# Kernel tuning notes

Measured on AMD Instinct MI355X. Metric: run time of the kernel, lower is better.

## Reference

```python
import jax, jax.numpy as jnp
import numpy as np

T, D, E, K, F, SF = 4096, 1024, 8, 2, 1024, 1024  # tokens, d_model, experts, top_k, moe_ff, shared_ff


def setup_inputs() -> dict:
    key = jax.random.key(0)
    ks = jax.random.split(key, 10)
    hidden_states = jax.random.normal(ks[0], (T, D), jnp.float32)
    # balanced expert assignment: the fused kernel's get_split_sizes assumes tokens
    # split evenly across experts after permute_tokens, so exactly T*K/E per expert
    flat = jnp.arange(T * K) % E
    flat = jax.random.permutation(ks[1], flat)
    topk_indices = flat.reshape(T, K).astype(jnp.int32)
    w = jax.random.uniform(ks[2], (T, K), jnp.float32)
    topk_weights = w / w.sum(-1, keepdims=True)  # norm_topk_prob
    s = 0.02
    w_gate = jax.random.normal(ks[3], (E, D, F), jnp.float32) * s
    w_up = jax.random.normal(ks[4], (E, D, F), jnp.float32) * s
    w_down = jax.random.normal(ks[5], (E, F, D), jnp.float32) * s
    sw_gate = jax.random.normal(ks[6], (D, SF), jnp.float32) * s
    sw_up = jax.random.normal(ks[7], (D, SF), jnp.float32) * s
    sw_down = jax.random.normal(ks[8], (SF, D), jnp.float32) * s
    shared_gate_w = jax.random.normal(ks[9], (D, 1), jnp.float32) * s
    return dict(hidden_states=hidden_states, topk_weights=topk_weights,
                w_gate=w_gate, w_up=w_up, w_down=w_down,
                sw_gate=sw_gate, sw_up=sw_up, sw_down=sw_down,
                shared_gate_w=shared_gate_w, topk_indices=topk_indices)


def _silu(x):
    return x * jax.nn.sigmoid(x)


def reference(hidden_states, topk_weights, w_gate, w_up, w_down,
              sw_gate, sw_up, sw_down, shared_gate_w, topk_indices):
    t, d = hidden_states.shape
    e = w_gate.shape[0]
    k = topk_indices.shape[1]
    c = (t * k) // e  # tokens per expert (balanced split, as in get_split_sizes)

    # permute_tokens: replicate each token top_k times and sort by expert id
    flat_idx = topk_indices.reshape(-1)                    # [t*k]
    order = jnp.argsort(flat_idx)                          # dispatch permutation
    x_rep = jnp.repeat(hidden_states, k, axis=0)           # [t*k, d]
    xs = x_rep[order].reshape(e, c, d)                     # grouped per-expert

    # per-expert gated MLP (grouped GEMMs)
    h = _silu(jnp.einsum('ecd,edf->ecf', xs, w_gate)) * jnp.einsum('ecd,edf->ecf', xs, w_up)
    y = jnp.einsum('ecf,efd->ecd', h, w_down).reshape(t * k, d)

    # unpermute_tokens + weighted combine over top_k
    y = y[jnp.argsort(order)].reshape(t, k, d)
    out = (y * topk_weights[..., None]).sum(axis=1)        # [t, d]

    # shared expert with sigmoid gate
    s = jnp.einsum('tf,fd->td', _silu(hidden_states @ sw_gate) * (hidden_states @ sw_up), sw_down)
    g = jax.nn.sigmoid(hidden_states @ shared_gate_w)      # [t, 1]
    return (out + g * s).astype(hidden_states.dtype)
```

## Files before the change

### kernel.cpp

```cpp
#include <hip/hip_runtime.h>
#include <hip/hip_bf16.h>
#include <cstdint>
#include <cstddef>

#define TTOK 4096
#define DM   1024
#define NE   8
#define KTOP 2
#define FFD  1024
#define CPER 1024
#define MROWS 12288


typedef __attribute__((ext_vector_type(8))) short frag8;
typedef __attribute__((ext_vector_type(4))) float f32x4;

static __device__ __forceinline__ unsigned short f2bf(float f) {
  unsigned int u = __float_as_uint(f);
  u += 0x7fff + ((u >> 16) & 1);
  return (unsigned short)(u >> 16);
}
static __device__ __forceinline__ float bf2f(unsigned short u) {
  return __uint_as_float((unsigned int)u << 16);
}

static __device__ __forceinline__ void gld_lds16(const unsigned short* g, unsigned short* l) {
  __builtin_amdgcn_global_load_lds(
      (const __attribute__((address_space(1))) unsigned int*)g,
      (__attribute__((address_space(3))) unsigned int*)l,
      16, 0, 0);
}

static __device__ __forceinline__ int lds_slot64(int r, int c) {
  return r * 8 + (c ^ (r & 7));
}

static __device__ __forceinline__ void stage_tile64(const unsigned short* __restrict__ src,
                                                    int row0, int k0,
                                                    unsigned short* lds, int tid) {
#pragma unroll
  for (int it = 0; it < 4; ++it) {
    int seg = it * 256 + tid;
    int r = seg >> 3;
    int cs = (seg & 7) ^ (r & 7);
    gld_lds16(src + (size_t)(row0 + r) * 1024 + k0 + cs * 8, lds + seg * 8);
  }
}

static __device__ __forceinline__ void swizzle_xy(int& x, int& y) {
  int L = blockIdx.y * 8 + blockIdx.x;
  int xcd = L & 7;
  int s = L >> 3;
  y = xcd * 12 + s % 12;
  x = s / 12;
}

static __device__ __forceinline__ void swizzle_xy4(int& x, int& y) {
  int L = blockIdx.y * 4 + blockIdx.x;
  int xcd = L & 7;
  int s = L >> 3;
  y = xcd * 12 + s % 12;
  x = s / 12;
}

__global__ void prep_transw_kernel(
    const float* __restrict__ wg, const float* __restrict__ wu,
    const float* __restrict__ wd, const float* __restrict__ sg,
    const float* __restrict__ su, const float* __restrict__ sd,
    unsigned short* __restrict__ owg, unsigned short* __restrict__ owu,
    unsigned short* __restrict__ owd,
    const float* __restrict__ x, const float* __restrict__ gw,
    const int* __restrict__ idx, const float* __restrict__ tw,
    int* __restrict__ cnt, int* __restrict__ rowsrc,
    float* __restrict__ rowscale, unsigned short* __restrict__ xb) {
  int z = blockIdx.z;
  if (z == 27) {
    int bid = blockIdx.y * 16 + blockIdx.x;
    if (bid < 32) {
      int i = bid * 256 + threadIdx.x;
      int e = idx[i];
      int pos = atomicAdd(&cnt[e], 1);
      int j = e * CPER + pos;
      rowsrc[j] = i >> 1;
      rowscale[j] = tw[i];
      if (i < TTOK) rowsrc[8192 + i] = i;
    }
    int wave = threadIdx.x >> 6;
    int lane = threadIdx.x & 63;
    const float4* wr = (const float4*)gw;
#pragma unroll
    for (int s = 0; s < 4; ++s) {
      int row = bid * 16 + wave * 4 + s;
      const float4* xr = (const float4*)(x + (size_t)row * 1024);
      ushort4* ob = (ushort4*)(xb + (size_t)row * 1024);
      float acc = 0.f;
#pragma unroll
      for (int c = 0; c < 4; ++c) {
        int k = lane + 64 * c;
        float4 v = xr[k];
        float4 g = wr[k];
        acc += v.x * g.x + v.y * g.y + v.z * g.z + v.w * g.w;
        ushort4 o;
        o.x = f2bf(v.x); o.y = f2bf(v.y); o.z = f2bf(v.z); o.w = f2bf(v.w);
        ob[k] = o;
      }
#pragma unroll
      for (int off = 32; off; off >>= 1) acc += __shfl_down(acc, off);
      if (lane == 0) rowscale[8192 + row] = 1.f / (1.f + __expf(-acc));
    }
    return;
  }
  const float* src; unsigned short* dst;
  if (z < 8)       { src = wg + (size_t)z * 1048576;        dst = owg + (size_t)z * 1048576; }
  else if (z < 16) { src = wu + (size_t)(z - 8) * 1048576;  dst = owu + (size_t)(z - 8) * 1048576; }
  else if (z < 24) { src = wd + (size_t)(z - 16) * 1048576; dst = owd + (size_t)(z - 16) * 1048576; }
  else if (z == 24){ src = sg; dst = owg + (size_t)8 * 1048576; }
  else if (z == 25){ src = su; dst = owu + (size_t)8 * 1048576; }
  else             { src = sd; dst = owd + (size_t)8 * 1048576; }
  __shared__ float tile[64][65];
  int bx = blockIdx.x * 64;
  int by = blockIdx.y * 64;
  int c4 = threadIdx.x & 15;
  int r0 = threadIdx.x >> 4;
#pragma unroll
  for (int i = 0; i < 4; ++i) {
    int r = r0 + 16 * i;
    float4 v = *(const float4*)&src[(size_t)(by + r) * 1024 + bx + c4 * 4];
    tile[r][c4 * 4 + 0] = v.x; tile[r][c4 * 4 + 1] = v.y;
    tile[r][c4 * 4 + 2] = v.z; tile[r][c4 * 4 + 3] = v.w;
  }
  __syncthreads();
#pragma unroll
  for (int i = 0; i < 4; ++i) {
    int f = r0 + 16 * i;
    ushort4 o;
    o.x = f2bf(tile[c4 * 4 + 0][f]);
    o.y = f2bf(tile[c4 * 4 + 1][f]);
    o.z = f2bf(tile[c4 * 4 + 2][f]);
    o.w = f2bf(tile[c4 * 4 + 3][f]);
    *(ushort4*)&dst[(size_t)(bx + f) * 1024 + by + c4 * 4] = o;
  }
}

static __device__ __forceinline__ int eid_of(int y) { return (y < 64) ? (y >> 3) : 8; }

__global__ __launch_bounds__(256, 2) void gemm1_kernel(
    const unsigned short* __restrict__ A, const int* __restrict__ rowsrc,
    const unsigned short* __restrict__ Bg, const unsigned short* __restrict__ Bu,
    unsigned short* __restrict__ H) {
  __shared__ __align__(16) unsigned short As[128 * 64];
  __shared__ __align__(16) unsigned short Bgs[128 * 64];
  __shared__ __align__(16) unsigned short Bus[128 * 64];
  int tid = threadIdx.x;
  int bx, by;
  swizzle_xy(bx, by);
  int e = eid_of(by);
  int row0 = by * 128;
  int col0 = bx * 128;
  const unsigned short* Bge = Bg + (size_t)e * 1048576;
  const unsigned short* Bue = Bu + (size_t)e * 1048576;

  const unsigned short* pA[4];
#pragma unroll
  for (int it = 0; it < 4; ++it) {
    int seg = it * 256 + tid;
    int r = seg >> 3;
    int cs = (seg & 7) ^ (r & 7);
    pA[it] = A + (size_t)rowsrc[row0 + r] * 1024 + cs * 8;
  }

  int wave = tid >> 6, lane = tid & 63;
  int wm = wave >> 1, wn = wave & 1;
  int lr = lane & 15, q = lane >> 4;

  f32x4 accg[4][4], accu[4][4];
#pragma unroll
  for (int i = 0; i < 4; ++i)
#pragma unroll
    for (int j = 0; j < 4; ++j) {
      accg[i][j] = (f32x4){0.f, 0.f, 0.f, 0.f};
      accu[i][j] = (f32x4){0.f, 0.f, 0.f, 0.f};
    }

  for (int kt = 0; kt < 1024; kt += 64) {
#pragma unroll
    for (int it = 0; it < 4; ++it)
      gld_lds16(pA[it] + kt, As + (it * 256 + tid) * 8);
    stage_tile64(Bge, col0, kt, Bgs, tid);
    stage_tile64(Bue, col0, kt, Bus, tid);
    __syncthreads();
#pragma unroll
    for (int kk = 0; kk < 2; ++kk) {
      int c = kk * 4 + q;
      frag8 a[4], b0[4], b1[4];
#pragma unroll
      for (int i = 0; i < 4; ++i) {
        int r = wm * 64 + i * 16 + lr;
        a[i] = *(const frag8*)&As[lds_slot64(r, c) * 8];
      }
#pragma unroll
      for (int j = 0; j < 4; ++j) {
        int r = wn * 64 + j * 16 + lr;
        b0[j] = *(const frag8*)&Bgs[lds_slot64(r, c) * 8];
        b1[j] = *(const frag8*)&Bus[lds_slot64(r, c) * 8];
      }
#pragma unroll
      for (int i = 0; i < 4; ++i)
#pragma unroll
        for (int j = 0; j < 4; ++j) {
          accg[i][j] = __builtin_amdgcn_mfma_f32_16x16x32_bf16(a[i], b0[j], accg[i][j], 0, 0, 0);
          accu[i][j] = __builtin_amdgcn_mfma_f32_16x16x32_bf16(a[i], b1[j], accu[i][j], 0, 0, 0);
        }
    }
    __syncthreads();
  }
#pragma unroll
  for (int i = 0; i < 4; ++i)
#pragma unroll
    for (int j = 0; j < 4; ++j)
#pragma unroll
      for (int r = 0; r < 4; ++r) {
        int m = row0 + wm * 64 + i * 16 + q * 4 + r;
        int n = col0 + wn * 64 + j * 16 + lr;
        float gv = accg[i][j][r];
        float hv = gv / (1.f + __expf(-gv)) * accu[i][j][r];
        H[(size_t)m * 1024 + n] = f2bf(hv);
      }
}

__global__ __launch_bounds__(256, 2) void gemm2_kernel(
    const unsigned short* __restrict__ A, const unsigned short* __restrict__ B,
    const float* __restrict__ rowscale, const int* __restrict__ rowsrc,
    float* __restrict__ out) {
  __shared__ __align__(16) unsigned short As[128 * 64];
  __shared__ __align__(16) unsigned short Bs[256 * 64];
  int tid = threadIdx.x;
  int bx, by;
  swizzle_xy4(bx, by);
  int e = eid_of(by);
  int row0 = by * 128;
  int col0 = bx * 256;
  const unsigned short* Be = B + (size_t)e * 1048576;

  int wave = tid >> 6, lane = tid & 63;
  int wm = wave >> 1, wn = wave & 1;
  int lr = lane & 15, q = lane >> 4;

  f32x4 acc[4][8];
#pragma unroll
  for (int i = 0; i < 4; ++i)
#pragma unroll
    for (int j = 0; j < 8; ++j) acc[i][j] = (f32x4){0.f, 0.f, 0.f, 0.f};

  for (int kt = 0; kt < 1024; kt += 64) {
    stage_tile64(A, row0, kt, As, tid);
#pragma unroll
    for (int it = 0; it < 8; ++it) {
      int seg = it * 256 + tid;
      int r = seg >> 3;
      int cs = (seg & 7) ^ (r & 7);
      gld_lds16(Be + (size_t)(col0 + r) * 1024 + kt + cs * 8, Bs + seg * 8);
    }
    __syncthreads();
#pragma unroll
    for (int kk = 0; kk < 2; ++kk) {
      int c = kk * 4 + q;
      frag8 a[4], b[8];
#pragma unroll
      for (int i = 0; i < 4; ++i) {
        int r = wm * 64 + i * 16 + lr;
        a[i] = *(const frag8*)&As[lds_slot64(r, c) * 8];
      }
#pragma unroll
      for (int j = 0; j < 8; ++j) {
        int r = wn * 128 + j * 16 + lr;
        b[j] = *(const frag8*)&Bs[lds_slot64(r, c) * 8];
      }
#pragma unroll
      for (int i = 0; i < 4; ++i)
#pragma unroll
        for (int j = 0; j < 8; ++j)
          acc[i][j] = __builtin_amdgcn_mfma_f32_16x16x32_bf16(a[i], b[j], acc[i][j], 0, 0, 0);
    }
    __syncthreads();
  }
#pragma unroll
  for (int i = 0; i < 4; ++i)
#pragma unroll
    for (int r = 0; r < 4; ++r) {
      int m = row0 + wm * 64 + i * 16 + q * 4 + r;
      float sc = rowscale[m];
      float* orow = out + (size_t)rowsrc[m] * 1024;
#pragma unroll
      for (int j = 0; j < 8; ++j) {
        int n = col0 + wn * 128 + j * 16 + lr;
        atomicAdd(orow + n, sc * acc[i][j][r]);
      }
    }
}

extern "C" void kernel_launch(void* const* d_in, const int* in_sizes, int n_in,
                              void* d_out, int out_size, void* d_ws, size_t ws_size,
                              hipStream_t stream) {
  (void)in_sizes; (void)n_in; (void)out_size; (void)ws_size;
  const float* hidden  = (const float*)d_in[0];
  const float* topk_w  = (const float*)d_in[1];
  const float* w_gate  = (const float*)d_in[2];
  const float* w_up    = (const float*)d_in[3];
  const float* w_down  = (const float*)d_in[4];
  const float* sw_gate = (const float*)d_in[5];
  const float* sw_up   = (const float*)d_in[6];
  const float* sw_down = (const float*)d_in[7];
  const float* sgw     = (const float*)d_in[8];
  const int*   topk_i  = (const int*)d_in[9];
  float* out = (float*)d_out;

  char* p = (char*)d_ws;
  auto alloc = [&](size_t bytes) {
    char* r = p;
    p += (bytes + 255) & ~(size_t)255;
    return r;
  };
  unsigned short* Wg_all = (unsigned short*)alloc((size_t)9 * 1048576 * 2);
  unsigned short* Wu_all = (unsigned short*)alloc((size_t)9 * 1048576 * 2);
  unsigned short* Wd_all = (unsigned short*)alloc((size_t)9 * 1048576 * 2);
  unsigned short* Xbf    = (unsigned short*)alloc((size_t)TTOK * 1024 * 2);
  unsigned short* Hall   = (unsigned short*)alloc((size_t)MROWS * 1024 * 2);
  int*   cnt      = (int*)alloc(NE * 4);
  int*   rowsrc   = (int*)alloc((size_t)MROWS * 4);
  float* rowscale = (float*)alloc((size_t)MROWS * 4);

  hipMemsetAsync(cnt, 0, NE * 4, stream);
  hipMemsetAsync(out, 0, (size_t)TTOK * DM * 4, stream);

  prep_transw_kernel<<<dim3(16, 16, 28), 256, 0, stream>>>(
      w_gate, w_up, w_down, sw_gate, sw_up, sw_down, Wg_all, Wu_all, Wd_all,
      hidden, sgw, topk_i, topk_w, cnt, rowsrc, rowscale, Xbf);

  gemm1_kernel<<<dim3(8, 96), 256, 0, stream>>>(Xbf, rowsrc, Wg_all, Wu_all, Hall);
  gemm2_kernel<<<dim3(4, 96), 256, 0, stream>>>(Hall, Wd_all, rowscale, rowsrc, out);
}
```

Before: 310.0 us.

## Replace gemm2 atomic scatter with bf16 staging, grid barrier, and gather-combine

Gemm2 no longer does fp32 atomicAdds into the output. Each block writes scaled results as bf16 into a staging buffer, then all blocks meet at a software grid barrier on a counter. After the barrier they gather the two expert rows and the shared row per token, sum them, and store the output directly, so the output memset is dropped. This adds an inverse-permutation array, extra bf16 rounding of partial results, and a spin barrier that assumes all 384 blocks are resident at once, which risks deadlock if they are not.

```diff
diff --git a/kernel.cpp b/kernel.cpp
--- a/kernel.cpp
+++ b/kernel.cpp
@@ -10,6 +10,7 @@
 #define FFD  1024
 #define CPER 1024
 #define MROWS 12288
+#define G2BLK 384
 
 
 typedef __attribute__((ext_vector_type(8))) short frag8;
@@ -71,7 +72,7 @@
     unsigned short* __restrict__ owd,
     const float* __restrict__ x, const float* __restrict__ gw,
     const int* __restrict__ idx, const float* __restrict__ tw,
-    int* __restrict__ cnt, int* __restrict__ rowsrc,
+    int* __restrict__ cnt, int* __restrict__ rowsrc, int* __restrict__ inv,
     float* __restrict__ rowscale, unsigned short* __restrict__ xb) {
   int z = blockIdx.z;
   if (z == 27) {
@@ -83,6 +84,7 @@
       int j = e * CPER + pos;
       rowsrc[j] = i >> 1;
       rowscale[j] = tw[i];
+      inv[i] = j;
       if (i < TTOK) rowsrc[8192 + i] = i;
     }
     int wave = threadIdx.x >> 6;
@@ -230,8 +232,9 @@
 
 __global__ __launch_bounds__(256, 2) void gemm2_kernel(
     const unsigned short* __restrict__ A, const unsigned short* __restrict__ B,
-    const float* __restrict__ rowscale, const int* __restrict__ rowsrc,
-    float* __restrict__ out) {
+    const float* __restrict__ rowscale, unsigned short* __restrict__ Y,
+    const int* __restrict__ inv, float* __restrict__ out,
+    int* __restrict__ bar) {
   __shared__ __align__(16) unsigned short As[128 * 64];
   __shared__ __align__(16) unsigned short Bs[256 * 64];
   int tid = threadIdx.x;
@@ -290,13 +293,37 @@
     for (int r = 0; r < 4; ++r) {
       int m = row0 + wm * 64 + i * 16 + q * 4 + r;
       float sc = rowscale[m];
-      float* orow = out + (size_t)rowsrc[m] * 1024;
 #pragma unroll
       for (int j = 0; j < 8; ++j) {
         int n = col0 + wn * 128 + j * 16 + lr;
-        atomicAdd(orow + n, sc * acc[i][j][r]);
-      }
-    }
+        Y[(size_t)m * 1024 + n] = f2bf(sc * acc[i][j][r]);
+      }
+    }
+
+  __threadfence();
+  __syncthreads();
+  if (tid == 0) {
+    atomicAdd(bar, 1);
+    while (atomicAdd(bar, 0) < G2BLK) {}
+  }
+  __syncthreads();
+  __threadfence();
+
+  int gid = (blockIdx.y * 4 + blockIdx.x) * 256 + tid;
+  for (int slot = gid; slot < TTOK * 256; slot += G2BLK * 256) {
+    int t = slot >> 8;
+    int c = slot & 255;
+    int j0 = inv[2 * t], j1 = inv[2 * t + 1];
+    ushort4 a = ((const ushort4*)(Y + (size_t)j0 * 1024))[c];
+    ushort4 b = ((const ushort4*)(Y + (size_t)j1 * 1024))[c];
+    ushort4 s = ((const ushort4*)(Y + (size_t)(8192 + t) * 1024))[c];
+    float4 o;
+    o.x = bf2f(a.x) + bf2f(b.x) + bf2f(s.x);
+    o.y = bf2f(a.y) + bf2f(b.y) + bf2f(s.y);
+    o.z = bf2f(a.z) + bf2f(b.z) + bf2f(s.z);
+    o.w = bf2f(a.w) + bf2f(b.w) + bf2f(s.w);
+    ((float4*)(out + (size_t)t * 1024))[c] = o;
+  }
 }
 
 extern "C" void kernel_launch(void* const* d_in, const int* in_sizes, int n_in,
@@ -326,17 +353,19 @@
   unsigned short* Wd_all = (unsigned short*)alloc((size_t)9 * 1048576 * 2);
   unsigned short* Xbf    = (unsigned short*)alloc((size_t)TTOK * 1024 * 2);
   unsigned short* Hall   = (unsigned short*)alloc((size_t)MROWS * 1024 * 2);
-  int*   cnt      = (int*)alloc(NE * 4);
+  unsigned short* Yall   = (unsigned short*)alloc((size_t)MROWS * 1024 * 2);
+  int*   cnt      = (int*)alloc(16 * 4);
   int*   rowsrc   = (int*)alloc((size_t)MROWS * 4);
+  int*   inv      = (int*)alloc((size_t)TTOK * KTOP * 4);
   float* rowscale = (float*)alloc((size_t)MROWS * 4);
 
-  hipMemsetAsync(cnt, 0, NE * 4, stream);
-  hipMemsetAsync(out, 0, (size_t)TTOK * DM * 4, stream);
+  hipMemsetAsync(cnt, 0, 16 * 4, stream);
 
   prep_transw_kernel<<<dim3(16, 16, 28), 256, 0, stream>>>(
       w_gate, w_up, w_down, sw_gate, sw_up, sw_down, Wg_all, Wu_all, Wd_all,
-      hidden, sgw, topk_i, topk_w, cnt, rowsrc, rowscale, Xbf);
+      hidden, sgw, topk_i, topk_w, cnt, rowsrc, inv, rowscale, Xbf);
 
   gemm1_kernel<<<dim3(8, 96), 256, 0, stream>>>(Xbf, rowsrc, Wg_all, Wu_all, Hall);
-  gemm2_kernel<<<dim3(4, 96), 256, 0, stream>>>(Hall, Wd_all, rowscale, rowsrc, out);
-}
+  gemm2_kernel<<<dim3(4, 96), 256, 0, stream>>>(Hall, Wd_all, rowscale, Yall,
+                                                inv, out, cnt + 8);
+}
```

Result: slower. 388.7 us (+25.4%).
